# Kernel tuning notes

Measured on AMD Instinct MI355X. Metric: run time of the kernel, lower is better.

Reference implementation:

```python
import jax, jax.numpy as jnp
import numpy as np

B, V, C, M, CM, D, OUT = 16, 16, 64, 32, 16, 128, 600
VOCAB = {"cond": 4000, "proc": 2000, "drug": 600, "lab_item": 700, "lab_value": 2000, "inj_item": 400, "inj_value": 2000}


def _gru(x, Wih, Whh, bih, bhh):
    """Batch-first torch-style GRU. x: [N,T,D] -> (outputs [N,T,D], h_T [N,D])."""
    Dh = Whh.shape[1]

    def step(h, xt):
        gi = xt @ Wih.T + bih
        gh = h @ Whh.T + bhh
        ir, iz, ig = jnp.split(gi, 3, axis=-1)
        hr, hz, hg = jnp.split(gh, 3, axis=-1)
        r = jax.nn.sigmoid(ir + hr)
        z = jax.nn.sigmoid(iz + hz)
        n = jnp.tanh(ig + r * hg)
        h = (1.0 - z) * n + z * h
        return h, h

    h0 = jnp.zeros((x.shape[0], Dh), x.dtype)
    hT, ys = jax.lax.scan(step, h0, jnp.swapaxes(x, 0, 1))
    return jnp.swapaxes(ys, 0, 1), hT


def _hetero_mp(feats, Wself, Wmsg):
    """Heterogeneous message passing over node types on the fully-connected
    monitor<->visit-feature bipartite pattern: each node type combines a self
    transform with a transformed mean of the other node types, then ReLU.
    feats: list of [N,D]; Wself/Wmsg: [T,D,D]."""
    stacked = jnp.stack(feats)  # [T,N,D]
    total = jnp.sum(stacked, axis=0)
    T = stacked.shape[0]
    outs = []
    for t in range(T):
        others = (total - stacked[t]) / (T - 1)
        outs.append(jax.nn.relu(stacked[t] @ Wself[t] + others @ Wmsg[t]))
    return outs


def _forward(codes_cond, codes_proc, codes_drug, codes_lab_item, codes_lab_value,
             codes_inj_item, codes_inj_value, weight, age,
             emb_cond, emb_proc, emb_drug, emb_lab_item, emb_lab_value,
             emb_inj_item, emb_inj_value,
             mgru_Wih, mgru_Whh, mgru_bih, mgru_bhh,
             vgru_Wih, vgru_Whh, vgru_bih, vgru_bhh,
             gnn_Wself, gnn_Wmsg,
             fc_weight_W, fc_weight_b, fc_age_W, fc_age_b,
             fc_patient_W, fc_patient_b):
    # ---- visit-event features: embedding lookup + sum-pool over codes ----
    vis = {}
    for k, codes, emb in (("cond", codes_cond, emb_cond),
                          ("proc", codes_proc, emb_proc),
                          ("drug", codes_drug, emb_drug)):
        vis[k] = jnp.sum(emb[codes], axis=2)  # [B,V,D]
    visit_keys = ("cond", "proc", "drug")

    # ---- monitor-event pairs: (item * value) embeddings, GNN, two-level GRU ----
    pairs = (
        (codes_lab_item, codes_lab_value, emb_lab_item, emb_lab_value, "lab_item", (0, 2, 3, 4)),
        (codes_inj_item, codes_inj_value, emb_inj_item, emb_inj_value, "inj_item", (1, 2, 3, 4)),
    )
    hid = {}
    for p, (ci, cv, ei, ev, ikey, gidx) in enumerate(pairs):
        mon = jnp.sum(ei[ci] * ev[cv], axis=3)  # [B,V,M,D]
        feats = [mon.reshape(-1, D)]  # monitor node type, [B*V*M, D]
        for k in visit_keys:  # visit features repeated across monitors
            feats.append(jnp.broadcast_to(vis[k][:, :, None, :], (B, V, M, D)).reshape(-1, D))
        outs = _hetero_mp(feats, gnn_Wself[p], gnn_Wmsg[p])
        for t, k in enumerate((ikey,) + visit_keys):
            g = gidx[t]
            # monitor-level GRU over the M monitors of each visit
            o, _ = _gru(outs[t].reshape(B * V, M, D), mgru_Wih[g], mgru_Whh[g], mgru_bih[g], mgru_bhh[g])
            last = o[:, -1, :].reshape(B, V, D)  # last monitor state per visit
            # visit-level GRU (source uses visit_gru[feature_key1] for all keys)
            _, h = _gru(last, vgru_Wih[p], vgru_Whh[p], vgru_bih[p], vgru_bhh[p])
            hid[k] = h if k not in hid else hid[k] + h

    # ---- weight / age scalar features ----
    for k, x, W, b, vi in (("weight", weight, fc_weight_W, fc_weight_b, 2),
                           ("age", age, fc_age_W, fc_age_b, 3)):
        mask = (x != 0.0)[..., None]  # [B,V,1]
        xe = (x[..., None] * W[:, 0] + b) * mask  # Linear(1->D) then zero-mask
        _, h = _gru(xe, vgru_Wih[vi], vgru_Whh[vi], vgru_bih[vi], vgru_bhh[vi])
        hid[k] = h

    # ---- concat in dict-insertion order, then ReLU + Linear head ----
    pe = jnp.concatenate([hid["lab_item"], hid["cond"], hid["proc"], hid["drug"],
                          hid["inj_item"], hid["weight"], hid["age"]], axis=-1)  # [B, 7D]
    return jax.nn.relu(pe) @ fc_patient_W.T + fc_patient_b  # [B, OUT]


def setup_inputs() -> dict:
    key = jax.random.key(0)
    ks = iter(jax.random.split(key, 64))

    def nrm(shape, s=0.1):
        return (jax.random.normal(next(ks), shape) * s).astype(jnp.float32)

    def emb_table(vsz):
        t = nrm((vsz, D), 1.0)
        return t.at[0].set(0.0)  # padding_idx=0 row is zero

    inp = {}
    inp["codes_cond"] = jax.random.randint(next(ks), (B, V, C), 0, VOCAB["cond"], dtype=jnp.int32)
    inp["codes_proc"] = jax.random.randint(next(ks), (B, V, C), 0, VOCAB["proc"], dtype=jnp.int32)
    inp["codes_drug"] = jax.random.randint(next(ks), (B, V, C), 0, VOCAB["drug"], dtype=jnp.int32)
    inp["codes_lab_item"] = jax.random.randint(next(ks), (B, V, M, CM), 0, VOCAB["lab_item"], dtype=jnp.int32)
    inp["codes_lab_value"] = jax.random.randint(next(ks), (B, V, M, CM), 0, VOCAB["lab_value"], dtype=jnp.int32)
    inp["codes_inj_item"] = jax.random.randint(next(ks), (B, V, M, CM), 0, VOCAB["inj_item"], dtype=jnp.int32)
    inp["codes_inj_value"] = jax.random.randint(next(ks), (B, V, M, CM), 0, VOCAB["inj_value"], dtype=jnp.int32)
    inp["weight"] = jax.random.uniform(next(ks), (B, V), minval=0.1, maxval=1.0, dtype=jnp.float32)
    inp["age"] = jax.random.uniform(next(ks), (B, V), minval=0.1, maxval=1.0, dtype=jnp.float32)
    inp["emb_cond"] = emb_table(VOCAB["cond"])
    inp["emb_proc"] = emb_table(VOCAB["proc"])
    inp["emb_drug"] = emb_table(VOCAB["drug"])
    inp["emb_lab_item"] = emb_table(VOCAB["lab_item"])
    inp["emb_lab_value"] = emb_table(VOCAB["lab_value"])
    inp["emb_inj_item"] = emb_table(VOCAB["inj_item"])
    inp["emb_inj_value"] = emb_table(VOCAB["inj_value"])
    inp["mgru_Wih"] = nrm((5, 3 * D, D))
    inp["mgru_Whh"] = nrm((5, 3 * D, D))
    inp["mgru_bih"] = nrm((5, 3 * D))
    inp["mgru_bhh"] = nrm((5, 3 * D))
    inp["vgru_Wih"] = nrm((4, 3 * D, D))
    inp["vgru_Whh"] = nrm((4, 3 * D, D))
    inp["vgru_bih"] = nrm((4, 3 * D))
    inp["vgru_bhh"] = nrm((4, 3 * D))
    inp["gnn_Wself"] = nrm((2, 4, D, D))
    inp["gnn_Wmsg"] = nrm((2, 4, D, D))
    inp["fc_weight_W"] = nrm((D, 1))
    inp["fc_weight_b"] = nrm((D,))
    inp["fc_age_W"] = nrm((D, 1))
    inp["fc_age_b"] = nrm((D,))
    inp["fc_patient_W"] = nrm((OUT, 7 * D))
    inp["fc_patient_b"] = nrm((OUT,))
    return inp


def reference(codes_cond, codes_proc, codes_drug, codes_lab_item, codes_lab_value,
              codes_inj_item, codes_inj_value, weight, age,
              emb_cond, emb_proc, emb_drug, emb_lab_item, emb_lab_value,
              emb_inj_item, emb_inj_value,
              mgru_Wih, mgru_Whh, mgru_bih, mgru_bhh,
              vgru_Wih, vgru_Whh, vgru_bih, vgru_bhh,
              gnn_Wself, gnn_Wmsg,
              fc_weight_W, fc_weight_b, fc_age_W, fc_age_b,
              fc_patient_W, fc_patient_b):
    return _forward(codes_cond, codes_proc, codes_drug, codes_lab_item, codes_lab_value,
                    codes_inj_item, codes_inj_value, weight, age,
                    emb_cond, emb_proc, emb_drug, emb_lab_item, emb_lab_value,
                    emb_inj_item, emb_inj_value,
                    mgru_Wih, mgru_Whh, mgru_bih, mgru_bhh,
                    vgru_Wih, vgru_Whh, vgru_bih, vgru_bhh,
                    gnn_Wself, gnn_Wmsg,
                    fc_weight_W, fc_weight_b, fc_age_W, fc_age_b,
                    fc_patient_W, fc_patient_b)
```

## Files before the change

### kernel.cpp

```cpp
#include <hip/hip_runtime.h>
#include <math.h>

#define B_   16
#define V_   16
#define C_   64
#define M_   32
#define CM_  16
#define D_   128
#define OUT_ 600
#define NSEQ 256
#define NROW 8192

typedef __attribute__((ext_vector_type(8))) short bf16x8;
typedef __attribute__((ext_vector_type(4))) short bf16x4;
typedef __attribute__((ext_vector_type(4))) float f32x4;
typedef __attribute__((ext_vector_type(2))) unsigned int u32x2;

__device__ __forceinline__ unsigned short f2bf(float x) {
  union { float f; unsigned u; } v; v.f = x;
  unsigned r = v.u + 0x7fff + ((v.u >> 16) & 1);
  return (unsigned short)(r >> 16);
}
__device__ __forceinline__ float bf2f(short s) {
  union { unsigned u; float f; } v;
  v.u = ((unsigned)(unsigned short)s) << 16;
  return v.f;
}
__device__ __forceinline__ float u2f(unsigned u) {
  union { unsigned u; float f; } v; v.u = u; return v.f;
}
__device__ __forceinline__ float fsig(float x)  { return __fdividef(1.f, 1.f + __expf(-x)); }
__device__ __forceinline__ float ftanh(float x) { return 1.f - 2.f*__fdividef(1.f, __expf(2.f*x) + 1.f); }

__device__ __forceinline__ void ldsbar() {
  asm volatile("s_waitcnt lgkmcnt(0)" ::: "memory");
  __builtin_amdgcn_s_barrier();
  asm volatile("" ::: "memory");
}

#define GLD(dst, ptr, offstr) \
  asm volatile("global_load_dwordx2 %0, %1, off offset:" offstr \
               : "=v"(dst) : "v"(ptr) : "memory")

constexpr int OFF_VIS   = 0;
constexpr int OFF_VISB  = 98304;
constexpr int OFF_MONB  = 147456;
constexpr int OFF_TOTB  = 1196032;
constexpr int OFF_W12T  = 2244608;
constexpr int OFF_WIHB  = 2375680;
constexpr int OFF_WIHTV = 2498560;
constexpr int OFF_XE    = 2695168;
constexpr int OFF_GI    = 2760704;
constexpr int OFF_LAST  = 27926528;
constexpr int OFF_VH    = 29171712;

__global__ __launch_bounds__(256) void k_prepvis(
    const float* __restrict__ Wself, const float* __restrict__ Wmsg,
    const float* __restrict__ mWih,  const float* __restrict__ vWih,
    const float* __restrict__ wgt,   const float* __restrict__ age,
    const float* __restrict__ fwW,   const float* __restrict__ fwB,
    const float* __restrict__ faW,   const float* __restrict__ faB,
    const int* __restrict__ cc, const int* __restrict__ cp, const int* __restrict__ cd,
    const float* __restrict__ ec, const float* __restrict__ ep, const float* __restrict__ ed,
    short* __restrict__ w12t, short* __restrict__ wihb,
    float* __restrict__ wihTv, float* __restrict__ xe,
    float* __restrict__ vis, short* __restrict__ visb)
{
  int bx = blockIdx.x, tid = threadIdx.x;
  if (bx < 1024) {
    int lin = bx*256 + tid;
    int pt = lin >> 15, rem = lin & 32767;
    int n = rem >> 8, k = rem & 255;
    float v;
    if (k < 128) v = Wself[pt*16384 + k*128 + n] - Wmsg[pt*16384 + k*128 + n]*(1.f/3.f);
    else         v = Wmsg[pt*16384 + (k-128)*128 + n]*(1.f/3.f);
    w12t[lin] = (short)f2bf(v);
  } else if (bx < 1984) {
    int lin = (bx-1024)*256 + tid;
    wihb[lin] = (short)f2bf(mWih[lin]);
  } else if (bx < 2752) {
    int lin = (bx-1984)*256 + tid;
    int g = lin / 49152, rem2 = lin % 49152;
    int k = rem2 / 384, j = rem2 % 384;
    wihTv[lin] = vWih[g*49152 + j*128 + k];
  } else if (bx < 3008) {
    int lin = (bx-2752)*256 + tid;
    int which = lin >> 15, rem2 = lin & 32767;
    int n = rem2 >> 7, d = rem2 & 127;
    float x  = which ? age[n] : wgt[n];
    float Wv = which ? faW[d] : fwW[d];
    float bb = which ? faB[d] : fwB[d];
    xe[lin] = (x != 0.0f) ? (x*Wv + bb) : 0.0f;
  } else {
    int idx = (bx-3008)*256 + tid;
    int type = idx >> 15;
    int r = idx & 32767;
    int bv = r >> 7, d = r & 127;
    const int*   codes = (type==0) ? cc : (type==1) ? cp : cd;
    const float* emb   = (type==0) ? ec : (type==1) ? ep : ed;
    float acc = 0.f;
    for (int c = 0; c < C_; ++c) {
      int code = codes[bv*C_ + c];
      acc += emb[code*D_ + d];
    }
    vis [(type*NSEQ + bv)*D_ + d] = acc;
    visb[(type*NSEQ + bv)*D_ + d] = (short)f2bf(acc);
  }
}

__global__ __launch_bounds__(128) void k_mon(
    const int* __restrict__ cli, const int* __restrict__ clv,
    const int* __restrict__ cii, const int* __restrict__ civ,
    const float* __restrict__ eli, const float* __restrict__ elv,
    const float* __restrict__ eii, const float* __restrict__ eiv,
    const float* __restrict__ vis,
    short* __restrict__ monb, short* __restrict__ totb)
{
  int p   = blockIdx.x >> 13;
  int bvm = blockIdx.x & 8191;
  int d   = threadIdx.x;
  const int* ci = p ? cii : cli;  const int* cv = p ? civ : clv;
  const float* ei = p ? eii : eli; const float* ev = p ? eiv : elv;
  float acc = 0.f;
  #pragma unroll
  for (int c = 0; c < CM_; ++c) {
    int iv = ci[bvm*CM_ + c];
    int vv = cv[bvm*CM_ + c];
    acc += ei[iv*D_ + d] * ev[vv*D_ + d];
  }
  int bv = bvm >> 5;
  float vsum = vis[bv*D_ + d] + vis[(NSEQ + bv)*D_ + d] + vis[(2*NSEQ + bv)*D_ + d];
  monb[(p*NROW + bvm)*D_ + d] = (short)f2bf(acc);
  totb[(p*NROW + bvm)*D_ + d] = (short)f2bf(acc + vsum);
}

__global__ __launch_bounds__(256, 4) void k_gg(
    const short* __restrict__ monb, const short* __restrict__ totb,
    const short* __restrict__ visb, const short* __restrict__ w12t,
    const short* __restrict__ wihb, const float* __restrict__ mbih,
    short* __restrict__ gi)
{
  const int pt = blockIdx.x >> 6;
  const int rb = blockIdx.x & 63;
  const int p = pt >> 2, t = pt & 3;
  const int g = (pt % 4 == 0) ? (pt / 4) : (pt % 4 + 1);
  const int row0 = rb * 128;
  const int tid = threadIdx.x;
  const int w = tid >> 6, lane = tid & 63;
  const int c = lane & 15, q = lane >> 4;

  __shared__ short smem[2*128*72];
  short (*Xs)[72]  = (short(*)[72])smem;
  short (*Ws)[72]  = (short(*)[72])(smem + 128*72);
  short (*Ys)[136] = (short(*)[136])smem;
  float (*giS)[68] = (float(*)[68])smem;

  const int rowL = tid >> 1, kc = tid & 1;
  const int rowG = row0 + rowL;
  const int bv = rowG >> 5;
  const int mg = w >> 1, ng = w & 1;

  f32x4 acc1[4][4];
  #pragma unroll
  for (int mi = 0; mi < 4; ++mi)
    #pragma unroll
    for (int ni = 0; ni < 4; ++ni) acc1[mi][ni] = (f32x4){0.f,0.f,0.f,0.f};

  const short* featp = (t == 0) ? (monb + ((size_t)p*NROW + rowG)*128)
                                : (visb + ((size_t)(t-1)*NSEQ + bv)*128);
  const short* totp  = totb + ((size_t)p*NROW + rowG)*128;
  const short* wrow  = w12t + ((size_t)pt*128 + rowL)*256;

  #pragma unroll 1
  for (int ks = 0; ks < 4; ++ks) {
    __syncthreads();
    int kg = ks*64 + kc*32;
    const short* srcX = (kg < 128) ? (featp + kg) : (totp + (kg - 128));
    const short* srcW = wrow + kg;
    short* dX = &Xs[rowL][kc*32];
    short* dW = &Ws[rowL][kc*32];
    #pragma unroll
    for (int i = 0; i < 4; ++i) {
      *(bf16x8*)(dX + 8*i) = *(const bf16x8*)(srcX + 8*i);
      *(bf16x8*)(dW + 8*i) = *(const bf16x8*)(srcW + 8*i);
    }
    __syncthreads();
    #pragma unroll
    for (int kk = 0; kk < 2; ++kk) {
      bf16x8 af[4], bfr[4];
      #pragma unroll
      for (int mi = 0; mi < 4; ++mi)
        af[mi] = *(const bf16x8*)&Xs[(mg*4+mi)*16 + c][kk*32 + q*8];
      #pragma unroll
      for (int ni = 0; ni < 4; ++ni)
        bfr[ni] = *(const bf16x8*)&Ws[(ng*4+ni)*16 + c][kk*32 + q*8];
      #pragma unroll
      for (int mi = 0; mi < 4; ++mi)
        #pragma unroll
        for (int ni = 0; ni < 4; ++ni)
          acc1[mi][ni] = __builtin_amdgcn_mfma_f32_16x16x32_bf16(af[mi], bfr[ni], acc1[mi][ni], 0, 0, 0);
    }
  }
  __syncthreads();

  #pragma unroll
  for (int mi = 0; mi < 4; ++mi)
    #pragma unroll
    for (int ni = 0; ni < 4; ++ni)
      #pragma unroll
      for (int reg = 0; reg < 4; ++reg)
        Ys[(mg*4+mi)*16 + q*4 + reg][(ng*4+ni)*16 + c] =
            (short)f2bf(fmaxf(acc1[mi][ni][reg], 0.f));
  __syncthreads();

  bf16x8 Af[2][4];
  #pragma unroll
  for (int mi = 0; mi < 2; ++mi)
    #pragma unroll
    for (int kt = 0; kt < 4; ++kt)
      Af[mi][kt] = *(const bf16x8*)&Ys[(w*2+mi)*16 + c][kt*32 + q*8];

  float bihv[24];
  #pragma unroll
  for (int nt = 0; nt < 24; ++nt)
    bihv[nt] = mbih[g*384 + nt*16 + c];

  short* gslab = gi + (((size_t)pt*64 + rb)*32)*384*4;
  #pragma unroll 1
  for (int cn = 0; cn < 6; ++cn) {
    f32x4 acc2[2][4];
    #pragma unroll
    for (int mi = 0; mi < 2; ++mi)
      #pragma unroll
      for (int ni = 0; ni < 4; ++ni) acc2[mi][ni] = (f32x4){0.f,0.f,0.f,0.f};
    #pragma unroll
    for (int ni = 0; ni < 4; ++ni) {
      int n = (cn*4 + ni)*16 + c;
      const short* bp_ = wihb + ((size_t)g*384 + n)*128 + q*8;
      #pragma unroll
      for (int kt = 0; kt < 4; ++kt) {
        bf16x8 bfr = *(const bf16x8*)(bp_ + kt*32);
        #pragma unroll
        for (int mi = 0; mi < 2; ++mi)
          acc2[mi][ni] = __builtin_amdgcn_mfma_f32_16x16x32_bf16(Af[mi][kt], bfr, acc2[mi][ni], 0, 0, 0);
      }
    }
    __syncthreads();
    #pragma unroll
    for (int mi = 0; mi < 2; ++mi)
      #pragma unroll
      for (int ni = 0; ni < 4; ++ni) {
        float bia = bihv[cn*4+ni];
        #pragma unroll
        for (int reg = 0; reg < 4; ++reg)
          giS[(w*2+mi)*16 + q*4 + reg][ni*16 + c] = acc2[mi][ni][reg] + bia;
      }
    __syncthreads();
    #pragma unroll
    for (int k = 0; k < 8; ++k) {
      int o4 = tid + k*256;
      int m = o4 >> 6, colL = o4 & 63;
      bf16x4 v;
      v[0] = (short)f2bf(giS[m][colL]);
      v[1] = (short)f2bf(giS[32+m][colL]);
      v[2] = (short)f2bf(giS[64+m][colL]);
      v[3] = (short)f2bf(giS[96+m][colL]);
      *(bf16x4*)&gslab[((size_t)m*384 + cn*64 + colL)*4] = v;
    }
  }
}

__global__ __launch_bounds__(512, 2) void k_mgru(
    const short* __restrict__ gi, const float* __restrict__ mWhh,
    const float* __restrict__ mbhh, float* __restrict__ last)
{
  const int run  = blockIdx.x >> 4;
  const int pair = blockIdx.x & 15;
  const int g = (run % 4 == 0) ? (run / 4) : (run % 4 + 1);
  const int tid = threadIdx.x;
  const int w = tid >> 6;
  const int lane = tid & 63;
  const int c = lane & 15, q = lane >> 4;
  const int j = w*16 + c;

  __shared__ short hb[2][4][16][40];

  for (int idx = tid; idx < 2*4*16*40; idx += 512)
    ((short*)hb)[idx] = 0;

  bf16x8 bfrag[3][4];
  #pragma unroll
  for (int gate = 0; gate < 3; ++gate) {
    const float* wp = mWhh + ((size_t)g*384 + gate*128 + j)*128 + q*8;
    #pragma unroll
    for (int kt = 0; kt < 4; ++kt) {
      float4 lo = *(const float4*)(wp + kt*32);
      float4 hi = *(const float4*)(wp + kt*32 + 4);
      bf16x8 t;
      t[0]=(short)f2bf(lo.x); t[1]=(short)f2bf(lo.y); t[2]=(short)f2bf(lo.z); t[3]=(short)f2bf(lo.w);
      t[4]=(short)f2bf(hi.x); t[5]=(short)f2bf(hi.y); t[6]=(short)f2bf(hi.z); t[7]=(short)f2bf(hi.w);
      bfrag[gate][kt] = t;
    }
  }
  const float bh0 = mbhh[g*384 +       j];
  const float bh1 = mbhh[g*384 + 128 + j];
  const float bh2 = mbhh[g*384 + 256 + j];

  const short* gib = gi + ((size_t)((run*64 + pair*4 + q)*32))*1536;
  const short* gpl = gib + j*4;

  float hf[4] = {0.f,0.f,0.f,0.f};
  const int ktw = w >> 1;
  const int kkw = (w & 1)*16 + c;

  u32x2 g0[3], g1[3], g2[3];
  GLD(g0[0], gpl,        "0");
  GLD(g0[1], gpl,        "1024");
  GLD(g0[2], gpl,        "2048");
  GLD(g1[0], gpl + 1536, "0");
  GLD(g1[1], gpl + 1536, "1024");
  GLD(g1[2], gpl + 1536, "2048");
  const short* gpn = gpl + 2*1536;

  ldsbar();

  auto step = [&](int m, u32x2 (&gcur)[3], u32x2 (&giss)[3], int wsel) {
    const int cur = m & 1, nxt = cur ^ 1;
    bf16x8 a[4];
    #pragma unroll
    for (int kt = 0; kt < 4; ++kt)
      a[kt] = *(const bf16x8*)&hb[cur][kt][c][q*8];
    f32x4 acc[3];
    #pragma unroll
    for (int gate = 0; gate < 3; ++gate) {
      f32x4 t = {0.f,0.f,0.f,0.f};
      #pragma unroll
      for (int kt = 0; kt < 4; ++kt)
        t = __builtin_amdgcn_mfma_f32_16x16x32_bf16(a[kt], bfrag[gate][kt], t, 0, 0, 0);
      acc[gate] = t;
    }
    if (wsel == 0) {
      GLD(giss[0], gpn, "0");
      GLD(giss[1], gpn, "1024");
      GLD(giss[2], gpn, "2048");
      gpn += 1536;
    }
    if (wsel == 0)      asm volatile("s_waitcnt vmcnt(6)" ::: "memory");
    else if (wsel == 1) asm volatile("s_waitcnt vmcnt(3)" ::: "memory");
    else                asm volatile("s_waitcnt vmcnt(0)" ::: "memory");
    __builtin_amdgcn_sched_barrier(0);
    float ga[3][4];
    #pragma unroll
    for (int gate = 0; gate < 3; ++gate) {
      ga[gate][0] = u2f(gcur[gate].x << 16);
      ga[gate][1] = u2f(gcur[gate].x & 0xffff0000u);
      ga[gate][2] = u2f(gcur[gate].y << 16);
      ga[gate][3] = u2f(gcur[gate].y & 0xffff0000u);
    }
    #pragma unroll
    for (int reg = 0; reg < 4; ++reg) {
      float rr = fsig(acc[0][reg] + bh0 + ga[0][reg]);
      float zz = fsig(acc[1][reg] + bh1 + ga[1][reg]);
      float nn = ftanh(ga[2][reg] + rr*(acc[2][reg] + bh2));
      float hnew = (1.f - zz)*nn + zz*hf[reg];
      hf[reg] = hnew;
      hb[nxt][ktw][q*4 + reg][kkw] = (short)f2bf(hnew);
    }
    ldsbar();
  };

  #pragma unroll 1
  for (int mb = 0; mb < 30; mb += 6) {
    step(mb+0, g0, g2, 0);
    step(mb+1, g1, g0, 0);
    step(mb+2, g2, g1, 0);
    step(mb+3, g0, g2, 0);
    step(mb+4, g1, g0, 0);
    step(mb+5, g2, g1, 0);
  }
  step(30, g0, g2, 1);
  step(31, g1, g0, 2);

  #pragma unroll
  for (int reg = 0; reg < 4; ++reg)
    last[((size_t)run*NSEQ + pair*16 + q*4 + reg)*D_ + j] = hf[reg];
}

__global__ __launch_bounds__(768) void k_vgru(
    const float* __restrict__ last, const float* __restrict__ xe,
    const float* __restrict__ wihTv, const float* __restrict__ vbih,
    const float* __restrict__ vWhh, const float* __restrict__ vbhh,
    float* __restrict__ vh)
{
  int run = blockIdx.x >> 4, b = blockIdx.x & 15;
  int tid = threadIdx.x;
  int vidx = (run < 4) ? 0 : (run < 8) ? 1 : (run - 6);

  __shared__ float Xs[16][128];
  __shared__ float giL[16*384];
  __shared__ __align__(16) float hsv[128];
  __shared__ float gh[384];

  const float* X = (run < 8) ? (last + ((size_t)run*NSEQ + b*16)*D_)
                             : (xe + ((size_t)(run-8)*NSEQ + b*16)*D_);
  for (int idx = tid; idx < 2048; idx += 768)
    ((float*)Xs)[idx] = X[idx];
  if (tid < 128) hsv[tid] = 0.f;
  __syncthreads();

  {
    int half = (tid >= 384) ? 1 : 0;
    int j = tid - half*384;
    float accv[8];
    float bias = vbih[vidx*384 + j];
    #pragma unroll
    for (int s = 0; s < 8; ++s) accv[s] = bias;
    const float* W = wihTv + vidx*49152 + j;
    #pragma unroll 4
    for (int k = 0; k < 128; ++k) {
      float wv = W[k*384];
      #pragma unroll
      for (int s = 0; s < 8; ++s) accv[s] += Xs[half*8 + s][k] * wv;
    }
    #pragma unroll
    for (int s = 0; s < 8; ++s)
      giL[(half*8 + s)*384 + j] = accv[s];
  }

  int j = tid >> 1, kh = tid & 1;
  float w[64];
  const float4* wrow = (const float4*)(vWhh + (vidx*384 + j)*128 + kh*64);
  #pragma unroll
  for (int k4 = 0; k4 < 16; ++k4) {
    float4 t4 = wrow[k4];
    w[4*k4] = t4.x; w[4*k4+1] = t4.y; w[4*k4+2] = t4.z; w[4*k4+3] = t4.w;
  }
  float bj = vbhh[vidx*384 + j];
  __syncthreads();

  #pragma unroll 1
  for (int v = 0; v < 16; ++v) {
    const float4* h4 = (const float4*)(hsv + kh*64);
    float p0 = 0.f, p1 = 0.f;
    #pragma unroll
    for (int k4 = 0; k4 < 8; ++k4) {
      float4 u0 = h4[k4], u1 = h4[k4+8];
      p0 += w[4*k4   ]*u0.x + w[4*k4+1 ]*u0.y + w[4*k4+2 ]*u0.z + w[4*k4+3 ]*u0.w;
      p1 += w[4*k4+32]*u1.x + w[4*k4+33]*u1.y + w[4*k4+34]*u1.z + w[4*k4+35]*u1.w;
    }
    float part = p0 + p1;
    part += __shfl_xor(part, 1);
    if (kh == 0) gh[j] = bj + ((j < 256) ? giL[v*384 + j] : 0.f) + part;
    __syncthreads();
    if (tid < 128) {
      float r = fsig(gh[tid]);
      float z = fsig(gh[tid+128]);
      float gin = giL[v*384 + 256 + tid];
      float n = ftanh(gin + r*gh[tid+256]);
      hsv[tid] = (1.f - z)*n + z*hsv[tid];
    }
    __syncthreads();
  }
  if (tid < 128) vh[(run*16 + b)*D_ + tid] = hsv[tid];
}

__global__ __launch_bounds__(256) void k_head(
    const float* __restrict__ vh, const float* __restrict__ Wp,
    const float* __restrict__ bp, float* __restrict__ out)
{
  const int o = blockIdx.x;
  const int tid = threadIdx.x;
  const int b = tid & 15, kc = tid >> 4;
  const int a1[7] = {0,1,2,3,4,8,9};
  const int a2[7] = {-1,5,6,7,-1,-1,-1};
  const float4* wb = (const float4*)(Wp + (size_t)o*896 + kc*56);
  float acc = 0.f;
  #pragma unroll
  for (int i = 0; i < 14; ++i) {
    int cc2 = kc*56 + i*4;
    int s = cc2 >> 7, d0 = cc2 & 127;
    float4 a = *(const float4*)(vh + (a1[s]*16 + b)*D_ + d0);
    int s2 = a2[s];
    if (s2 >= 0) {
      float4 a2v = *(const float4*)(vh + (s2*16 + b)*D_ + d0);
      a.x += a2v.x; a.y += a2v.y; a.z += a2v.z; a.w += a2v.w;
    }
    a.x = fmaxf(a.x, 0.f); a.y = fmaxf(a.y, 0.f);
    a.z = fmaxf(a.z, 0.f); a.w = fmaxf(a.w, 0.f);
    float4 ww = wb[i];
    acc += a.x*ww.x + a.y*ww.y + a.z*ww.z + a.w*ww.w;
  }
  __shared__ float red[16][17];
  red[kc][b] = acc;
  __syncthreads();
  if (tid < 16) {
    float s = 0.f;
    #pragma unroll
    for (int k = 0; k < 16; ++k) s += red[k][tid];
    out[tid*OUT_ + o] = s + bp[o];
  }
}

extern "C" void kernel_launch(void* const* d_in, const int* in_sizes, int n_in,
                              void* d_out, int out_size, void* d_ws, size_t ws_size,
                              hipStream_t stream)
{
  (void)in_sizes; (void)n_in; (void)out_size; (void)ws_size;
  const int*   cc   = (const int*)  d_in[0];
  const int*   cp   = (const int*)  d_in[1];
  const int*   cd   = (const int*)  d_in[2];
  const int*   cli  = (const int*)  d_in[3];
  const int*   clv  = (const int*)  d_in[4];
  const int*   cii  = (const int*)  d_in[5];
  const int*   civ  = (const int*)  d_in[6];
  const float* wgt  = (const float*)d_in[7];
  const float* age  = (const float*)d_in[8];
  const float* ec   = (const float*)d_in[9];
  const float* ep   = (const float*)d_in[10];
  const float* ed   = (const float*)d_in[11];
  const float* eli  = (const float*)d_in[12];
  const float* elv  = (const float*)d_in[13];
  const float* eii  = (const float*)d_in[14];
  const float* eiv  = (const float*)d_in[15];
  const float* mWih = (const float*)d_in[16];
  const float* mWhh = (const float*)d_in[17];
  const float* mbih = (const float*)d_in[18];
  const float* mbhh = (const float*)d_in[19];
  const float* vWih = (const float*)d_in[20];
  const float* vWhh = (const float*)d_in[21];
  const float* vbih = (const float*)d_in[22];
  const float* vbhh = (const float*)d_in[23];
  const float* Wself= (const float*)d_in[24];
  const float* Wmsg = (const float*)d_in[25];
  const float* fwW  = (const float*)d_in[26];
  const float* fwB  = (const float*)d_in[27];
  const float* faW  = (const float*)d_in[28];
  const float* faB  = (const float*)d_in[29];
  const float* Wp   = (const float*)d_in[30];
  const float* bp   = (const float*)d_in[31];
  float* out = (float*)d_out;
  float* ws  = (float*)d_ws;

  float* vis   = ws + OFF_VIS;
  short* visb  = (short*)(ws + OFF_VISB);
  short* monb  = (short*)(ws + OFF_MONB);
  short* totb  = (short*)(ws + OFF_TOTB);
  short* w12t  = (short*)(ws + OFF_W12T);
  short* wihb  = (short*)(ws + OFF_WIHB);
  float* wihTv = ws + OFF_WIHTV;
  float* xe    = ws + OFF_XE;
  short* gi    = (short*)(ws + OFF_GI);
  float* last  = ws + OFF_LAST;
  float* vh    = ws + OFF_VH;

  k_prepvis<<<3392, 256, 0, stream>>>(Wself, Wmsg, mWih, vWih, wgt, age,
                                      fwW, fwB, faW, faB,
                                      cc, cp, cd, ec, ep, ed,
                                      w12t, wihb, wihTv, xe, vis, visb);
  k_mon <<<16384, 128, 0, stream>>>(cli, clv, cii, civ, eli, elv, eii, eiv,
                                    vis, monb, totb);
  k_gg  <<<512, 256, 0, stream>>>(monb, totb, visb, w12t, wihb, mbih, gi);
  k_mgru<<<128, 512, 0, stream>>>(gi, mWhh, mbhh, last);
  k_vgru<<<160, 768, 0, stream>>>(last, xe, wihTv, vbih, vWhh, vbhh, vh);
  k_head<<<600, 256, 0, stream>>>(vh, Wp, bp, out);
}
```

Before: 266.9 us.

## Fuse visit GRU with output head via atomics and pair runs per block

```diff
diff --git a/kernel.cpp b/kernel.cpp
--- a/kernel.cpp
+++ b/kernel.cpp
@@ -62,9 +62,11 @@
     const float* __restrict__ faW,   const float* __restrict__ faB,
     const int* __restrict__ cc, const int* __restrict__ cp, const int* __restrict__ cd,
     const float* __restrict__ ec, const float* __restrict__ ep, const float* __restrict__ ed,
+    const float* __restrict__ bp,
     short* __restrict__ w12t, short* __restrict__ wihb,
     float* __restrict__ wihTv, float* __restrict__ xe,
-    float* __restrict__ vis, short* __restrict__ visb)
+    float* __restrict__ vis, short* __restrict__ visb,
+    float* __restrict__ outb)
 {
   int bx = blockIdx.x, tid = threadIdx.x;
   if (bx < 1024) {
@@ -91,7 +93,7 @@
     float Wv = which ? faW[d] : fwW[d];
     float bb = which ? faB[d] : fwB[d];
     xe[lin] = (x != 0.0f) ? (x*Wv + bb) : 0.0f;
-  } else {
+  } else if (bx < 3392) {
     int idx = (bx-3008)*256 + tid;
     int type = idx >> 15;
     int r = idx & 32767;
@@ -105,6 +107,9 @@
     }
     vis [(type*NSEQ + bv)*D_ + d] = acc;
     visb[(type*NSEQ + bv)*D_ + d] = (short)f2bf(acc);
+  } else {
+    int idx = (bx-3392)*256 + tid;
+    if (idx < B_*OUT_) outb[idx] = bp[idx % OUT_];
   }
 }
 
@@ -386,118 +391,111 @@
     last[((size_t)run*NSEQ + pair*16 + q*4 + reg)*D_ + j] = hf[reg];
 }
 
-__global__ __launch_bounds__(768) void k_vgru(
+__global__ __launch_bounds__(768, 1) void k_vgh(
     const float* __restrict__ last, const float* __restrict__ xe,
     const float* __restrict__ wihTv, const float* __restrict__ vbih,
     const float* __restrict__ vWhh, const float* __restrict__ vbhh,
-    float* __restrict__ vh)
+    const float* __restrict__ Wp, float* __restrict__ out)
 {
-  int run = blockIdx.x >> 4, b = blockIdx.x & 15;
-  int tid = threadIdx.x;
-  int vidx = (run < 4) ? 0 : (run < 8) ? 1 : (run - 6);
-
-  __shared__ float Xs[16][128];
-  __shared__ float giL[16*384];
-  __shared__ __align__(16) float hsv[128];
-  __shared__ float gh[384];
-
-  const float* X = (run < 8) ? (last + ((size_t)run*NSEQ + b*16)*D_)
-                             : (xe + ((size_t)(run-8)*NSEQ + b*16)*D_);
-  for (int idx = tid; idx < 2048; idx += 768)
-    ((float*)Xs)[idx] = X[idx];
-  if (tid < 128) hsv[tid] = 0.f;
+  const int s = blockIdx.x >> 4;
+  const int b = blockIdx.x & 15;
+  const int tid = threadIdx.x;
+  const int a1 = s + ((s >= 5) ? 3 : 0);
+  const bool haspair = (s >= 1 && s <= 3);
+  const int a2 = haspair ? (s + 4) : -1;
+  const int half = (tid >= 384) ? 1 : 0;
+  const int j = tid - half*384;
+  const int run = half ? a2 : a1;
+  const bool act = (run >= 0);
+  const int vidx = act ? ((run < 4) ? 0 : (run < 8) ? 1 : (run - 6)) : 0;
+
+  __shared__ float Xs[2][16][128];
+  __shared__ short giLb[2][16*384];
+  __shared__ __align__(16) float hsv[2][128];
+  __shared__ float gh[2][384];
+
+  if (act) {
+    const float* X = (run < 8) ? (last + ((size_t)run*NSEQ + b*16)*D_)
+                               : (xe + ((size_t)(run-8)*NSEQ + b*16)*D_);
+    for (int idx = j; idx < 2048; idx += 384)
+      ((float*)Xs[half])[idx] = X[idx];
+  }
+  if (tid < 256) hsv[tid>>7][tid&127] = 0.f;
   __syncthreads();
 
-  {
-    int half = (tid >= 384) ? 1 : 0;
-    int j = tid - half*384;
-    float accv[8];
-    float bias = vbih[vidx*384 + j];
-    #pragma unroll
-    for (int s = 0; s < 8; ++s) accv[s] = bias;
+  if (act) {
+    const float bias = vbih[vidx*384 + j];
     const float* W = wihTv + vidx*49152 + j;
-    #pragma unroll 4
-    for (int k = 0; k < 128; ++k) {
-      float wv = W[k*384];
-      #pragma unroll
-      for (int s = 0; s < 8; ++s) accv[s] += Xs[half*8 + s][k] * wv;
-    }
-    #pragma unroll
-    for (int s = 0; s < 8; ++s)
-      giL[(half*8 + s)*384 + j] = accv[s];
-  }
-
-  int j = tid >> 1, kh = tid & 1;
-  float w[64];
-  const float4* wrow = (const float4*)(vWhh + (vidx*384 + j)*128 + kh*64);
-  #pragma unroll
-  for (int k4 = 0; k4 < 16; ++k4) {
-    float4 t4 = wrow[k4];
-    w[4*k4] = t4.x; w[4*k4+1] = t4.y; w[4*k4+2] = t4.z; w[4*k4+3] = t4.w;
-  }
-  float bj = vbhh[vidx*384 + j];
+    #pragma unroll 1
+    for (int vh2 = 0; vh2 < 2; ++vh2) {
+      float accv[8];
+      #pragma unroll
+      for (int v = 0; v < 8; ++v) accv[v] = bias;
+      #pragma unroll 4
+      for (int k = 0; k < 128; ++k) {
+        float wv = W[k*384];
+        #pragma unroll
+        for (int v = 0; v < 8; ++v) accv[v] += Xs[half][vh2*8 + v][k] * wv;
+      }
+      #pragma unroll
+      for (int v = 0; v < 8; ++v)
+        giLb[half][(vh2*8 + v)*384 + j] = (short)f2bf(accv[v]);
+    }
+  }
+
+  float w[128];
+  float bj = 0.f;
+  if (act) {
+    const float4* wrow = (const float4*)(vWhh + ((size_t)vidx*384 + j)*128);
+    #pragma unroll
+    for (int k4 = 0; k4 < 32; ++k4) {
+      float4 t4 = wrow[k4];
+      w[4*k4] = t4.x; w[4*k4+1] = t4.y; w[4*k4+2] = t4.z; w[4*k4+3] = t4.w;
+    }
+    bj = vbhh[vidx*384 + j];
+  }
   __syncthreads();
 
   #pragma unroll 1
   for (int v = 0; v < 16; ++v) {
-    const float4* h4 = (const float4*)(hsv + kh*64);
-    float p0 = 0.f, p1 = 0.f;
-    #pragma unroll
-    for (int k4 = 0; k4 < 8; ++k4) {
-      float4 u0 = h4[k4], u1 = h4[k4+8];
-      p0 += w[4*k4   ]*u0.x + w[4*k4+1 ]*u0.y + w[4*k4+2 ]*u0.z + w[4*k4+3 ]*u0.w;
-      p1 += w[4*k4+32]*u1.x + w[4*k4+33]*u1.y + w[4*k4+34]*u1.z + w[4*k4+35]*u1.w;
-    }
-    float part = p0 + p1;
-    part += __shfl_xor(part, 1);
-    if (kh == 0) gh[j] = bj + ((j < 256) ? giL[v*384 + j] : 0.f) + part;
+    if (act) {
+      const float4* h4 = (const float4*)hsv[half];
+      float p0 = 0.f, p1 = 0.f;
+      #pragma unroll
+      for (int k4 = 0; k4 < 16; ++k4) {
+        float4 u0 = h4[k4], u1 = h4[k4+16];
+        p0 += w[4*k4   ]*u0.x + w[4*k4+1 ]*u0.y + w[4*k4+2 ]*u0.z + w[4*k4+3 ]*u0.w;
+        p1 += w[4*k4+64]*u1.x + w[4*k4+65]*u1.y + w[4*k4+66]*u1.z + w[4*k4+67]*u1.w;
+      }
+      gh[half][j] = bj + ((j < 256) ? bf2f(giLb[half][v*384 + j]) : 0.f) + p0 + p1;
+    }
     __syncthreads();
-    if (tid < 128) {
-      float r = fsig(gh[tid]);
-      float z = fsig(gh[tid+128]);
-      float gin = giL[v*384 + 256 + tid];
-      float n = ftanh(gin + r*gh[tid+256]);
-      hsv[tid] = (1.f - z)*n + z*hsv[tid];
+    if (tid < 256) {
+      const int h2 = tid >> 7, jj = tid & 127;
+      if (h2 == 0 || haspair) {
+        float r = fsig(gh[h2][jj]);
+        float z = fsig(gh[h2][jj+128]);
+        float gin = bf2f(giLb[h2][v*384 + 256 + jj]);
+        float n = ftanh(gin + r*gh[h2][jj+256]);
+        hsv[h2][jj] = (1.f - z)*n + z*hsv[h2][jj];
+      }
     }
     __syncthreads();
   }
-  if (tid < 128) vh[(run*16 + b)*D_ + tid] = hsv[tid];
-}
-
-__global__ __launch_bounds__(256) void k_head(
-    const float* __restrict__ vh, const float* __restrict__ Wp,
-    const float* __restrict__ bp, float* __restrict__ out)
-{
-  const int o = blockIdx.x;
-  const int tid = threadIdx.x;
-  const int b = tid & 15, kc = tid >> 4;
-  const int a1[7] = {0,1,2,3,4,8,9};
-  const int a2[7] = {-1,5,6,7,-1,-1,-1};
-  const float4* wb = (const float4*)(Wp + (size_t)o*896 + kc*56);
-  float acc = 0.f;
-  #pragma unroll
-  for (int i = 0; i < 14; ++i) {
-    int cc2 = kc*56 + i*4;
-    int s = cc2 >> 7, d0 = cc2 & 127;
-    float4 a = *(const float4*)(vh + (a1[s]*16 + b)*D_ + d0);
-    int s2 = a2[s];
-    if (s2 >= 0) {
-      float4 a2v = *(const float4*)(vh + (s2*16 + b)*D_ + d0);
-      a.x += a2v.x; a.y += a2v.y; a.z += a2v.z; a.w += a2v.w;
-    }
-    a.x = fmaxf(a.x, 0.f); a.y = fmaxf(a.y, 0.f);
-    a.z = fmaxf(a.z, 0.f); a.w = fmaxf(a.w, 0.f);
-    float4 ww = wb[i];
-    acc += a.x*ww.x + a.y*ww.y + a.z*ww.z + a.w*ww.w;
-  }
-  __shared__ float red[16][17];
-  red[kc][b] = acc;
-  __syncthreads();
-  if (tid < 16) {
-    float s = 0.f;
-    #pragma unroll
-    for (int k = 0; k < 16; ++k) s += red[k][tid];
-    out[tid*OUT_ + o] = s + bp[o];
+
+  if (tid < OUT_) {
+    const int o = tid;
+    const float* wr = Wp + (size_t)o*896 + s*128;
+    float acc = 0.f;
+    #pragma unroll
+    for (int d4 = 0; d4 < 32; ++d4) {
+      float4 ww  = *(const float4*)(wr + d4*4);
+      float4 h0v = *(const float4*)&hsv[0][d4*4];
+      float4 h1v = *(const float4*)&hsv[1][d4*4];
+      acc += fmaxf(h0v.x + h1v.x, 0.f)*ww.x + fmaxf(h0v.y + h1v.y, 0.f)*ww.y
+           + fmaxf(h0v.z + h1v.z, 0.f)*ww.z + fmaxf(h0v.w + h1v.w, 0.f)*ww.w;
+    }
+    atomicAdd(&out[b*OUT_ + o], acc);
   }
 }
 
@@ -551,16 +549,14 @@
   float* xe    = ws + OFF_XE;
   short* gi    = (short*)(ws + OFF_GI);
   float* last  = ws + OFF_LAST;
-  float* vh    = ws + OFF_VH;
-
-  k_prepvis<<<3392, 256, 0, stream>>>(Wself, Wmsg, mWih, vWih, wgt, age,
+
+  k_prepvis<<<3430, 256, 0, stream>>>(Wself, Wmsg, mWih, vWih, wgt, age,
                                       fwW, fwB, faW, faB,
-                                      cc, cp, cd, ec, ep, ed,
-                                      w12t, wihb, wihTv, xe, vis, visb);
+                                      cc, cp, cd, ec, ep, ed, bp,
+                                      w12t, wihb, wihTv, xe, vis, visb, out);
   k_mon <<<16384, 128, 0, stream>>>(cli, clv, cii, civ, eli, elv, eii, eiv,
                                     vis, monb, totb);
   k_gg  <<<512, 256, 0, stream>>>(monb, totb, visb, w12t, wihb, mbih, gi);
   k_mgru<<<128, 512, 0, stream>>>(gi, mWhh, mbhh, last);
-  k_vgru<<<160, 768, 0, stream>>>(last, xe, wihTv, vbih, vWhh, vbhh, vh);
-  k_head<<<600, 256, 0, stream>>>(vh, Wp, bp, out);
-}
+  k_vgh <<<112, 768, 0, stream>>>(last, xe, wihTv, vbih, vWhh, vbhh, Wp, out);
+}
```

Measured after the change: 419.8 us. +57.3%, slower.
